# Performance work log

Measured on AMD Instinct MI355X. Metric: run time of the kernel, lower is better.

Reference implementation:

```python
import jax, jax.numpy as jnp
from jax import lax
import numpy as np

LOGZERO = -(65504.0 ** 2)  # -torch.finfo(float16).min**2


def setup_inputs() -> dict:
    key = jax.random.key(0)
    ks = jax.random.split(key, 5)
    B, T, D, V, CB, Ly = 32, 512, 512, 4096, 30, 4
    x = jax.random.normal(ks[0], (B, T, D), jnp.float32)
    W = jax.random.normal(ks[1], (V, D), jnp.float32) * 0.02
    b = jax.random.normal(ks[2], (V,), jnp.float32) * 0.02
    xl = jnp.full((B,), T, jnp.int32)
    y = jax.random.randint(ks[3], (B, Ly), 1, V)  # partial hypothesis (last token used)
    # unique candidate ids per row (exclude blank=0) to avoid duplicate-scatter ambiguity
    scores = jax.random.uniform(ks[4], (B, V - 1))
    ctc_beam_idx = jnp.argsort(scores, axis=1)[:, :CB] + 1
    return {"x": x, "W": W, "b": b, "xl": xl, "y": y,
            "ctc_beam_idx": ctc_beam_idx, "blank": 0, "eos": V - 1}


def reference(x, W, b, xl, y, ctc_beam_idx, blank, eos):
    B, T, D = x.shape
    V = W.shape[0]
    CB = ctc_beam_idx.shape[1]
    # forward(): Linear + log_softmax  -> (B, T, V)
    logp = jax.nn.log_softmax(jnp.einsum("btd,vd->btv", x, W) + b, axis=-1)
    # preProcess(): lastP[1] = cumsum of blank logprob over time, lastP[0] = logzero
    blank_lp = logp[:, :, blank]                     # (B, T)
    lastP1 = jnp.cumsum(blank_lp, axis=1).T          # (T, B)
    lastP0 = jnp.full((T, B), LOGZERO, logp.dtype)
    lastPsum = jnp.logaddexp(lastP0, lastP1)         # (T, B)
    # cState.select / bState.select -> candidate and blank scores per beam hyp
    Xn = jnp.take_along_axis(logp, ctc_beam_idx[:, None, :], axis=2)  # (B, T, CB)
    Xn = Xn.transpose(1, 0, 2)                                        # (T, B, CB)
    Xb = jnp.broadcast_to(blank_lp.T[:, :, None], Xn.shape)           # (T, B, CB)
    # prefP: lastPsum everywhere, lastP[1] where candidate == last prediction
    same = (y[:, -1][:, None] == ctc_beam_idx)                        # (B, CB)
    prefP = jnp.where(same[None], lastP1[:, :, None], lastPsum[:, :, None])  # (T, B, CB)
    Ly = y.shape[1]
    start = min(Ly, T - 1)
    loop_start = max(start, 1)
    Pn0 = jnp.full((B, CB), LOGZERO, logp.dtype)
    Pb0 = jnp.full((B, CB), LOGZERO, logp.dtype)
    if start == 0:
        Pn0 = Xn[0]
    def step(carry, inp):
        Pn_prev, Pb_prev = carry
        pref_prev, xn_t, xb_t = inp
        Pn = jnp.logaddexp(Pn_prev, pref_prev) + xn_t
        Pb = jnp.logaddexp(Pn_prev, Pb_prev) + xb_t
        return (Pn, Pb), (Pn, Pb)
    _, (Pn_seq, Pb_seq) = lax.scan(
        step, (Pn0, Pb0),
        (prefP[loop_start - 1:T - 1], Xn[loop_start:], Xb[loop_start:]))
    if start == 0:  # prepend the preset t=0 entry
        Pn_seq = jnp.concatenate([Pn0[None], Pn_seq], axis=0)
        Pb_seq = jnp.concatenate([Pb0[None], Pb_seq], axis=0)
    # curP over t in [start, T)
    curP_t = jnp.logaddexp(Pn_seq, Pb_seq)                            # (T-start, B, CB)
    t_idx = jnp.arange(start, T)
    valid = xl[None, :] > t_idx[:, None]                              # (T-start, B)
    curP_t = jnp.where(valid[:, :, None], curP_t, LOGZERO)
    curP = jax.nn.logsumexp(curP_t, axis=0)                           # (B, CB)
    # scatter into vocab; initial self.prefP == 0.0
    finalP = jnp.full((B, V), LOGZERO, curP.dtype)
    finalP = finalP.at[jnp.arange(B)[:, None], ctc_beam_idx].set(curP)
    # eos score: lastPsum at final valid frame only
    ar = jnp.arange(T)
    maskBT = xl[:, None] > ar[None, :]
    mask0 = (xl - 1)[:, None] > ar[None, :]
    lps = jnp.where(maskBT & ~mask0, lastPsum.T, 0.0)                 # (B, T)
    finalP = finalP.at[:, eos].set(jnp.sum(lps, axis=1))
    finalP = finalP.at[:, blank].set(LOGZERO)
    return finalP
```

## Files before the change

### kernel.cpp

```cpp
#include <hip/hip_runtime.h>
#include <hip/hip_fp8.h>

#define LOGZERO -4290774016.0f
#define L2E 1.4426950408889634f
#define LN2 0.6931471805599453f

constexpr int Bb = 32, Tt = 512, Dd = 512, Vv = 4096;
constexpr int BT = Bb * Tt;

typedef __attribute__((ext_vector_type(4))) float f32x4;
typedef __attribute__((ext_vector_type(2))) long i64x2;
typedef long i64;

#define GLOBAL_AS __attribute__((address_space(1)))
#define LDS_AS    __attribute__((address_space(3)))

__device__ __forceinline__ float fexp2(float x) { return __builtin_amdgcn_exp2f(x); }
__device__ __forceinline__ float flog2(float x) { return __builtin_amdgcn_logf(x); }

__device__ __forceinline__ unsigned cvt4_fp8(float4 v, float s) {
#if __has_builtin(__builtin_amdgcn_cvt_pk_fp8_f32)
  int p = __builtin_amdgcn_cvt_pk_fp8_f32(v.x * s, v.y * s, 0, false);
  p = __builtin_amdgcn_cvt_pk_fp8_f32(v.z * s, v.w * s, p, true);
  return (unsigned)p;
#else
  unsigned b0 = __hip_cvt_float_to_fp8(v.x * s, __HIP_SATFINITE, __HIP_E4M3);
  unsigned b1 = __hip_cvt_float_to_fp8(v.y * s, __HIP_SATFINITE, __HIP_E4M3);
  unsigned b2 = __hip_cvt_float_to_fp8(v.z * s, __HIP_SATFINITE, __HIP_E4M3);
  unsigned b3 = __hip_cvt_float_to_fp8(v.w * s, __HIP_SATFINITE, __HIP_E4M3);
  return b0 | (b1 << 8) | (b2 << 16) | (b3 << 24);
#endif
}

__device__ __forceinline__ float lg2add(float a, float b) {
  float mx = fmaxf(a, b);
  float d  = fabsf(a - b);
  return mx + flog2(1.0f + fexp2(-d));
}

__global__ __launch_bounds__(256) void kPre(const float* __restrict__ x,
                                            const float* __restrict__ W,
                                            unsigned char* __restrict__ Xfp,
                                            unsigned char* __restrict__ Wp) {
  const int blk = blockIdx.x, tid = threadIdx.x;
  const int t = blk * 256 + tid;
  if (blk < 2048) {
    int quad = t & 3, ln15 = (t >> 2) & 15, rtp = (t >> 6) & 1;
    int ks = (t >> 7) & 15, tM = t >> 11;
    const float* p0 = x + (size_t)(tM * 64 + rtp * 32 + ln15) * Dd + ks * 32 + quad * 8;
    const float* p1 = p0 + 16 * Dd;
    uint4 o;
    o.x = cvt4_fp8(*(const float4*)p0, 1.0f);
    o.y = cvt4_fp8(*(const float4*)(p0 + 4), 1.0f);
    o.z = cvt4_fp8(*(const float4*)p1, 1.0f);
    o.w = cvt4_fp8(*(const float4*)(p1 + 4), 1.0f);
    size_t slot = (size_t)tM * 2048 + (ks * 2 + rtp) * 64 + quad * 16 + ln15;
    *(uint4*)(Xfp + slot * 16) = o;
  } else {
    int tt = t - 2048 * 256;
    int quad = tt & 3, ln15 = (tt >> 2) & 15, ctp = (tt >> 6) & 1;
    int ks = (tt >> 7) & 15, cb = tt >> 11;
    const float* p0 = W + (size_t)(cb * 64 + ctp * 32 + ln15) * Dd + ks * 32 + quad * 8;
    const float* p1 = p0 + 16 * Dd;
    uint4 o;
    o.x = cvt4_fp8(*(const float4*)p0, 16.0f);
    o.y = cvt4_fp8(*(const float4*)(p0 + 4), 16.0f);
    o.z = cvt4_fp8(*(const float4*)p1, 16.0f);
    o.w = cvt4_fp8(*(const float4*)(p1 + 4), 16.0f);
    size_t slot = (size_t)cb * 2048 + (ks * 2 + ctp) * 64 + quad * 16 + ln15;
    *(uint4*)(Wp + slot * 16) = o;
  }
}

__global__ __launch_bounds__(256, 4) void kA(const unsigned char* __restrict__ Xfp,
                                             const unsigned char* __restrict__ Wp,
                                             const float* __restrict__ bias,
                                             const int* __restrict__ beam,
                                             const int* __restrict__ blankp,
                                             float* __restrict__ Spart,
                                             float* __restrict__ selL,
                                             int CB) {
  __shared__ unsigned char Ald[32768];
  __shared__ float Spw[4][64];
  __shared__ int   selv[31];
  __shared__ float selb[31];

  const int tid = threadIdx.x;
  const int tileN = blockIdx.x & 15;
  const int tileM = blockIdx.x >> 4;
  const int row0 = tileM * 64, col0 = tileN * 256;
  const int bb = row0 >> 9;
  const int lane = tid & 63, w = tid >> 6;
  const int ln15 = lane & 15, quad = lane >> 4;

  if (tid < 31) {
    int v = (tid == 0) ? *blankp : beam[bb * CB + tid - 1];
    selv[tid] = v;
    selb[tid] = bias[v];
  }

  const unsigned char* src = Xfp + (size_t)tileM * 32768;
  #pragma unroll
  for (int i = 0; i < 8; ++i) {
    int off = (w * 8 + i) * 1024;
    __builtin_amdgcn_global_load_lds((const GLOBAL_AS void*)(src + off + lane * 16),
                                     (LDS_AS void*)(Ald + off), 16, 0, 0);
  }
  __syncthreads();

  const int colw = col0 + w * 64;
  const int cb = tileN * 4 + w;
  f32x4 acc[4][4];
  #pragma unroll
  for (int ct = 0; ct < 4; ++ct)
    #pragma unroll
    for (int rt = 0; rt < 4; ++rt) acc[ct][rt] = {0.f, 0.f, 0.f, 0.f};

  const unsigned char* wpB = Wp + (size_t)cb * 32768 + lane * 16;
  i64x2 bc[2];
  bc[0] = *(const i64x2*)(wpB);
  bc[1] = *(const i64x2*)(wpB + 1024);

  #pragma unroll
  for (int ks = 0; ks < 16; ++ks) {
    i64x2 af[2];
    #pragma unroll
    for (int rtp = 0; rtp < 2; ++rtp)
      af[rtp] = *(const i64x2*)&Ald[(ks * 2 + rtp) * 1024 + lane * 16];
    i64x2 bn[2];
    int ks2 = (ks < 15) ? (ks + 1) : 15;
    bn[0] = *(const i64x2*)(wpB + ks2 * 2048);
    bn[1] = *(const i64x2*)(wpB + ks2 * 2048 + 1024);
    #pragma unroll
    for (int ct = 0; ct < 4; ++ct)
      #pragma unroll
      for (int rt = 0; rt < 4; ++rt)
        acc[ct][rt] = __builtin_amdgcn_mfma_f32_16x16x32_fp8_fp8(
            af[rt >> 1][rt & 1], bc[ct >> 1][ct & 1], acc[ct][rt], 0, 0, 0);
    bc[0] = bn[0]; bc[1] = bn[1];
  }

  float bvl[4];
  #pragma unroll
  for (int ct = 0; ct < 4; ++ct)
    bvl[ct] = bias[colw + (ct >> 1) * 32 + (ct & 1) * 16 + ln15] * L2E;
  const float SC = 0.0625f * L2E;

  #pragma unroll
  for (int rt = 0; rt < 4; ++rt) {
    #pragma unroll
    for (int r = 0; r < 4; ++r) {
      float s = 0.f;
      #pragma unroll
      for (int ct = 0; ct < 4; ++ct) s += fexp2(acc[ct][rt][r] * SC + bvl[ct]);
      s += __shfl_xor(s, 1, 64);
      s += __shfl_xor(s, 2, 64);
      s += __shfl_xor(s, 4, 64);
      s += __shfl_xor(s, 8, 64);
      if (ln15 == 0)
        Spw[w][(rt >> 1) * 32 + (rt & 1) * 16 + quad * 4 + r] = s;
    }
  }
  __syncthreads();
  if (tid < 64) {
    float p = Spw[0][tid] + Spw[1][tid] + Spw[2][tid] + Spw[3][tid];
    Spart[(size_t)tileN * BT + row0 + tid] = p;
  }

  const int tbase = row0 & 511;
  #pragma unroll
  for (int ct = 0; ct < 4; ++ct) {
    for (int s = 0; s < 31; ++s) {
      int local = selv[s] - colw - (ct >> 1) * 32 - (ct & 1) * 16;
      if (local >= 0 && local < 16 && ln15 == local) {
        float bvs = selb[s];
        #pragma unroll
        for (int rt = 0; rt < 4; ++rt)
          #pragma unroll
          for (int r = 0; r < 4; ++r) {
            int t = tbase + (rt >> 1) * 32 + (rt & 1) * 16 + quad * 4 + r;
            selL[((size_t)bb * Tt + t) * 31 + s] = acc[ct][rt][r] * 0.0625f + bvs;
          }
      }
    }
  }
}

__global__ __launch_bounds__(256) void kC(const float* __restrict__ selL,
                                          const float* __restrict__ Spart,
                                          const int* __restrict__ xl,
                                          const int* __restrict__ beam,
                                          const int* __restrict__ blankp,
                                          const int* __restrict__ eosp,
                                          float* __restrict__ out,
                                          int Ly, int CB) {
  __shared__ float sl[Tt * 31];
  __shared__ float lgS[Tt];
  __shared__ float lastP1[Tt];
  __shared__ float blankLp[Tt];
  const int b = blockIdx.x, tid = threadIdx.x;

  for (int i = tid; i < Tt * 31; i += 256)
    sl[i] = selL[(size_t)b * Tt * 31 + i] * L2E;
  for (int tt = tid; tt < Tt; tt += 256) {
    float s = 0.f;
    #pragma unroll
    for (int n = 0; n < 16; ++n) s += Spart[(size_t)n * BT + b * Tt + tt];
    lgS[tt] = flog2(s);
  }
  __syncthreads();

  float* orow = out + (size_t)b * Vv;
  for (int i = tid; i < Vv; i += 256) orow[i] = LOGZERO;

  const int xlb = xl[b];
  float curP = LOGZERO;
  if (tid < 64) {
    const int lane = tid;
    float vloc[8];
    float run = 0.f;
    #pragma unroll
    for (int u = 0; u < 8; ++u) {
      int t = lane * 8 + u;
      float bl = sl[t * 31] - lgS[t];
      blankLp[t] = bl;
      run += bl;
      vloc[u] = run;
    }
    float inc = run;
    #pragma unroll
    for (int off = 1; off < 64; off <<= 1) {
      float o = __shfl_up(inc, off, 64);
      if (lane >= off) inc += o;
    }
    float excl = inc - run;
    #pragma unroll
    for (int u = 0; u < 8; ++u) lastP1[lane * 8 + u] = vloc[u] + excl;

    const int kk = (lane < CB) ? lane : (CB - 1);
    const float LOG2ZERO = LOGZERO * L2E;
    float Pn = LOG2ZERO, Pb = LOG2ZERO;
    float mrun = -3.0e38f, srun = 0.0f;
    int start = (Ly < Tt - 1) ? Ly : (Tt - 1);
    if (start == 0) {
      Pn = sl[1 + kk] - lgS[0];
      float vv = (0 < xlb) ? lg2add(Pn, Pb) : LOG2ZERO;
      float nm = fmaxf(mrun, vv);
      srun = srun * fexp2(mrun - nm) + fexp2(vv - nm);
      mrun = nm;
    }
    int t0 = (start > 1) ? start : 1;
    #pragma unroll 2
    for (int t = t0; t < Tt; ++t) {
      float xn = sl[t * 31 + 1 + kk] - lgS[t];
      float xb = blankLp[t];
      float pref = lastP1[t - 1];
      float Pn2 = lg2add(Pn, pref) + xn;
      float Pb2 = lg2add(Pn, Pb) + xb;
      Pn = Pn2; Pb = Pb2;
      float vv = (t < xlb) ? lg2add(Pn, Pb) : LOG2ZERO;
      float nm = fmaxf(mrun, vv);
      srun = srun * fexp2(mrun - nm) + fexp2(vv - nm);
      mrun = nm;
    }
    curP = (mrun + flog2(srun)) * LN2;
  }
  __syncthreads();

  if (tid < 64) {
    if (tid < CB) orow[beam[b * CB + tid]] = curP;
  }
  __syncthreads();
  if (tid == 0) {
    float eosv = (xlb >= 1) ? lastP1[xlb - 1] * LN2 : 0.0f;
    orow[*eosp] = eosv;
    orow[*blankp] = LOGZERO;
  }
}

extern "C" void kernel_launch(void* const* d_in, const int* in_sizes, int n_in,
                              void* d_out, int out_size, void* d_ws, size_t ws_size,
                              hipStream_t stream) {
  (void)n_in; (void)out_size; (void)ws_size;
  const float* x    = (const float*)d_in[0];
  const float* W    = (const float*)d_in[1];
  const float* bias = (const float*)d_in[2];
  const int* xl     = (const int*)d_in[3];
  const int* beam   = (const int*)d_in[5];
  const int* blankp = (const int*)d_in[6];
  const int* eosp   = (const int*)d_in[7];
  const int Ly = in_sizes[4] / Bb;
  const int CB = in_sizes[5] / Bb;

  float* Spart = (float*)d_ws;
  float* selL  = (float*)((char*)d_ws + (size_t)0x100000);
  unsigned char* Xfp = (unsigned char*)((char*)d_ws + (size_t)0x400000);
  unsigned char* Wp  = (unsigned char*)((char*)d_ws + (size_t)0xC00000);
  float* outf = (float*)d_out;

  kPre<<<2560, 256, 0, stream>>>(x, W, Xfp, Wp);
  kA<<<4096, 256, 0, stream>>>(Xfp, Wp, bias, beam, blankp, Spart, selL, CB);
  kC<<<Bb, 256, 0, stream>>>(selL, Spart, xl, beam, blankp, eosp, outf, Ly, CB);
}
```

Measured before the change: 221.3 us.

## Switch FP8 GEMM to 32x32x64 scaled MFMA with matching operand layout

Replaces the 16x16x32 FP8 MFMA tiles with the gfx950 block-scaled 32x32x64 f8f6f4 MFMA, using hardware scale exponents to undo the 16x weight prescale. The pre-pack kernel is rewritten to emit the new 32-row/64-k fragment layout, and the softmax-sum and candidate extraction epilogues are remapped to the 32x32 accumulator layout. The aim is fewer MFMA issues and higher matrix throughput per K step, at the cost of larger per-instruction operands and a more complex accumulator index mapping.

```diff
diff --git a/kernel.cpp b/kernel.cpp
--- a/kernel.cpp
+++ b/kernel.cpp
@@ -8,9 +8,10 @@
 constexpr int Bb = 32, Tt = 512, Dd = 512, Vv = 4096;
 constexpr int BT = Bb * Tt;
 
-typedef __attribute__((ext_vector_type(4))) float f32x4;
-typedef __attribute__((ext_vector_type(2))) long i64x2;
-typedef long i64;
+typedef __attribute__((ext_vector_type(4)))  float f32x4;
+typedef __attribute__((ext_vector_type(16))) float f32x16;
+typedef __attribute__((ext_vector_type(4)))  int   i32x4;
+typedef __attribute__((ext_vector_type(8)))  int   i32x8;
 
 #define GLOBAL_AS __attribute__((address_space(1)))
 #define LDS_AS    __attribute__((address_space(3)))
@@ -42,33 +43,32 @@
                                             const float* __restrict__ W,
                                             unsigned char* __restrict__ Xfp,
                                             unsigned char* __restrict__ Wp) {
-  const int blk = blockIdx.x, tid = threadIdx.x;
-  const int t = blk * 256 + tid;
-  if (blk < 2048) {
-    int quad = t & 3, ln15 = (t >> 2) & 15, rtp = (t >> 6) & 1;
-    int ks = (t >> 7) & 15, tM = t >> 11;
-    const float* p0 = x + (size_t)(tM * 64 + rtp * 32 + ln15) * Dd + ks * 32 + quad * 8;
-    const float* p1 = p0 + 16 * Dd;
+  const int t = blockIdx.x * 256 + threadIdx.x;
+  if (t < 524288) {
+    const int tM = t >> 11, s = t & 2047;
+    const int l = s & 63, h = (s >> 6) & 1, rt = (s >> 7) & 1, kb = s >> 8;
+    const int row = tM * 64 + rt * 32 + (l & 31);
+    const int col = kb * 64 + ((l >> 5) << 5) + h * 16;
+    const float* p = x + (size_t)row * Dd + col;
     uint4 o;
-    o.x = cvt4_fp8(*(const float4*)p0, 1.0f);
-    o.y = cvt4_fp8(*(const float4*)(p0 + 4), 1.0f);
-    o.z = cvt4_fp8(*(const float4*)p1, 1.0f);
-    o.w = cvt4_fp8(*(const float4*)(p1 + 4), 1.0f);
-    size_t slot = (size_t)tM * 2048 + (ks * 2 + rtp) * 64 + quad * 16 + ln15;
-    *(uint4*)(Xfp + slot * 16) = o;
+    o.x = cvt4_fp8(*(const float4*)p, 1.0f);
+    o.y = cvt4_fp8(*(const float4*)(p + 4), 1.0f);
+    o.z = cvt4_fp8(*(const float4*)(p + 8), 1.0f);
+    o.w = cvt4_fp8(*(const float4*)(p + 12), 1.0f);
+    *(uint4*)(Xfp + (size_t)t * 16) = o;
   } else {
-    int tt = t - 2048 * 256;
-    int quad = tt & 3, ln15 = (tt >> 2) & 15, ctp = (tt >> 6) & 1;
-    int ks = (tt >> 7) & 15, cb = tt >> 11;
-    const float* p0 = W + (size_t)(cb * 64 + ctp * 32 + ln15) * Dd + ks * 32 + quad * 8;
-    const float* p1 = p0 + 16 * Dd;
+    const int tt = t - 524288;
+    const int cb = tt >> 11, s = tt & 2047;
+    const int l = s & 63, h = (s >> 6) & 1, ct = (s >> 7) & 1, kb = s >> 8;
+    const int row = cb * 64 + ct * 32 + (l & 31);
+    const int col = kb * 64 + ((l >> 5) << 5) + h * 16;
+    const float* p = W + (size_t)row * Dd + col;
     uint4 o;
-    o.x = cvt4_fp8(*(const float4*)p0, 16.0f);
-    o.y = cvt4_fp8(*(const float4*)(p0 + 4), 16.0f);
-    o.z = cvt4_fp8(*(const float4*)p1, 16.0f);
-    o.w = cvt4_fp8(*(const float4*)(p1 + 4), 16.0f);
-    size_t slot = (size_t)cb * 2048 + (ks * 2 + ctp) * 64 + quad * 16 + ln15;
-    *(uint4*)(Wp + slot * 16) = o;
+    o.x = cvt4_fp8(*(const float4*)p, 16.0f);
+    o.y = cvt4_fp8(*(const float4*)(p + 4), 16.0f);
+    o.z = cvt4_fp8(*(const float4*)(p + 8), 16.0f);
+    o.w = cvt4_fp8(*(const float4*)(p + 12), 16.0f);
+    *(uint4*)(Wp + (size_t)tt * 16) = o;
   }
 }
 
@@ -91,7 +91,7 @@
   const int row0 = tileM * 64, col0 = tileN * 256;
   const int bb = row0 >> 9;
   const int lane = tid & 63, w = tid >> 6;
-  const int ln15 = lane & 15, quad = lane >> 4;
+  const int l31 = lane & 31, hi = lane >> 5;
 
   if (tid < 31) {
     int v = (tid == 0) ? *blankp : beam[bb * CB + tid - 1];
@@ -110,55 +110,72 @@
 
   const int colw = col0 + w * 64;
   const int cb = tileN * 4 + w;
-  f32x4 acc[4][4];
-  #pragma unroll
-  for (int ct = 0; ct < 4; ++ct)
-    #pragma unroll
-    for (int rt = 0; rt < 4; ++rt) acc[ct][rt] = {0.f, 0.f, 0.f, 0.f};
+
+  f32x16 acc[2][2];
+  #pragma unroll
+  for (int ct = 0; ct < 2; ++ct)
+    #pragma unroll
+    for (int rt = 0; rt < 2; ++rt)
+      #pragma unroll
+      for (int r = 0; r < 16; ++r) acc[ct][rt][r] = 0.f;
 
   const unsigned char* wpB = Wp + (size_t)cb * 32768 + lane * 16;
-  i64x2 bc[2];
-  bc[0] = *(const i64x2*)(wpB);
-  bc[1] = *(const i64x2*)(wpB + 1024);
-
-  #pragma unroll
-  for (int ks = 0; ks < 16; ++ks) {
-    i64x2 af[2];
-    #pragma unroll
-    for (int rtp = 0; rtp < 2; ++rtp)
-      af[rtp] = *(const i64x2*)&Ald[(ks * 2 + rtp) * 1024 + lane * 16];
-    i64x2 bn[2];
-    int ks2 = (ks < 15) ? (ks + 1) : 15;
-    bn[0] = *(const i64x2*)(wpB + ks2 * 2048);
-    bn[1] = *(const i64x2*)(wpB + ks2 * 2048 + 1024);
-    #pragma unroll
-    for (int ct = 0; ct < 4; ++ct)
+
+  i32x8 bc[2];
+  #pragma unroll
+  for (int ct = 0; ct < 2; ++ct) {
+    i32x4 lo = *(const i32x4*)(wpB + (ct * 2) * 1024);
+    i32x4 hx = *(const i32x4*)(wpB + (ct * 2 + 1) * 1024);
+    bc[ct] = __builtin_shufflevector(lo, hx, 0, 1, 2, 3, 4, 5, 6, 7);
+  }
+
+  #pragma unroll
+  for (int kb = 0; kb < 8; ++kb) {
+    i32x8 af[2];
+    #pragma unroll
+    for (int rt = 0; rt < 2; ++rt) {
+      i32x4 lo = *(const i32x4*)&Ald[(kb * 4 + rt * 2) * 1024 + lane * 16];
+      i32x4 hx = *(const i32x4*)&Ald[(kb * 4 + rt * 2 + 1) * 1024 + lane * 16];
+      af[rt] = __builtin_shufflevector(lo, hx, 0, 1, 2, 3, 4, 5, 6, 7);
+    }
+    i32x8 bn[2];
+    const int kn = (kb < 7) ? kb + 1 : 7;
+    #pragma unroll
+    for (int ct = 0; ct < 2; ++ct) {
+      i32x4 lo = *(const i32x4*)(wpB + (kn * 4 + ct * 2) * 1024);
+      i32x4 hx = *(const i32x4*)(wpB + (kn * 4 + ct * 2 + 1) * 1024);
+      bn[ct] = __builtin_shufflevector(lo, hx, 0, 1, 2, 3, 4, 5, 6, 7);
+    }
+    #pragma unroll
+    for (int ct = 0; ct < 2; ++ct)
       #pragma unroll
-      for (int rt = 0; rt < 4; ++rt)
-        acc[ct][rt] = __builtin_amdgcn_mfma_f32_16x16x32_fp8_fp8(
-            af[rt >> 1][rt & 1], bc[ct >> 1][ct & 1], acc[ct][rt], 0, 0, 0);
+      for (int rt = 0; rt < 2; ++rt)
+        acc[ct][rt] = __builtin_amdgcn_mfma_scale_f32_32x32x64_f8f6f4(
+            af[rt], bc[ct], acc[ct][rt],
+            0, 0,
+            0, 0x7f7f7f7f,
+            0, 0x7b7b7b7b);
     bc[0] = bn[0]; bc[1] = bn[1];
   }
 
-  float bvl[4];
-  #pragma unroll
-  for (int ct = 0; ct < 4; ++ct)
-    bvl[ct] = bias[colw + (ct >> 1) * 32 + (ct & 1) * 16 + ln15] * L2E;
-  const float SC = 0.0625f * L2E;
-
-  #pragma unroll
-  for (int rt = 0; rt < 4; ++rt) {
-    #pragma unroll
-    for (int r = 0; r < 4; ++r) {
-      float s = 0.f;
-      #pragma unroll
-      for (int ct = 0; ct < 4; ++ct) s += fexp2(acc[ct][rt][r] * SC + bvl[ct]);
+  float bvl[2];
+  #pragma unroll
+  for (int ct = 0; ct < 2; ++ct)
+    bvl[ct] = bias[colw + ct * 32 + l31] * L2E;
+
+  #pragma unroll
+  for (int rt = 0; rt < 2; ++rt) {
+    #pragma unroll
+    for (int reg = 0; reg < 16; ++reg) {
+      float s = fexp2(acc[0][rt][reg] * L2E + bvl[0]) +
+                fexp2(acc[1][rt][reg] * L2E + bvl[1]);
       s += __shfl_xor(s, 1, 64);
       s += __shfl_xor(s, 2, 64);
       s += __shfl_xor(s, 4, 64);
       s += __shfl_xor(s, 8, 64);
-      if (ln15 == 0)
-        Spw[w][(rt >> 1) * 32 + (rt & 1) * 16 + quad * 4 + r] = s;
+      s += __shfl_xor(s, 16, 64);
+      if (l31 == 0)
+        Spw[w][rt * 32 + (reg & 3) + 8 * (reg >> 2) + 4 * hi] = s;
     }
   }
   __syncthreads();
@@ -168,18 +185,18 @@
   }
 
   const int tbase = row0 & 511;
-  #pragma unroll
-  for (int ct = 0; ct < 4; ++ct) {
-    for (int s = 0; s < 31; ++s) {
-      int local = selv[s] - colw - (ct >> 1) * 32 - (ct & 1) * 16;
-      if (local >= 0 && local < 16 && ln15 == local) {
+  for (int s = 0; s < 31; ++s) {
+    int local = selv[s] - colw;
+    #pragma unroll
+    for (int ct = 0; ct < 2; ++ct) {
+      if (local >= ct * 32 && local < (ct + 1) * 32 && l31 == (local & 31)) {
         float bvs = selb[s];
         #pragma unroll
-        for (int rt = 0; rt < 4; ++rt)
+        for (int rt = 0; rt < 2; ++rt)
           #pragma unroll
-          for (int r = 0; r < 4; ++r) {
-            int t = tbase + (rt >> 1) * 32 + (rt & 1) * 16 + quad * 4 + r;
-            selL[((size_t)bb * Tt + t) * 31 + s] = acc[ct][rt][r] * 0.0625f + bvs;
+          for (int reg = 0; reg < 16; ++reg) {
+            int t = tbase + rt * 32 + (reg & 3) + 8 * (reg >> 2) + 4 * hi;
+            selL[((size_t)bb * Tt + t) * 31 + s] = acc[ct][rt][reg] + bvs;
           }
       }
     }
```

After: 325.0 us. 46.9% more time.
